# Kernel tuning notes

Hardware: AMD Instinct MI355X
Metric: run time of the kernel (lower is better)

Reference implementation:

```python
import jax, jax.numpy as jnp
import numpy as np

EMB = 1024
N_HEAD = 16
D_K = EMB // N_HEAD


def setup_inputs() -> dict:
    key = jax.random.key(0)
    ks = jax.random.split(key, 11)
    B, S = 4, 2048
    scale = 1.0 / np.sqrt(EMB)
    inp = {
        "q": jax.random.normal(ks[0], (B, S, EMB), jnp.float32),
        "k": jax.random.normal(ks[1], (B, S, EMB), jnp.float32),
        "v": jax.random.normal(ks[2], (B, S, EMB), jnp.float32),
        "Wq": jax.random.normal(ks[3], (EMB, EMB), jnp.float32) * scale,
        "bq": jnp.zeros((EMB,), jnp.float32),
        "Wk": jax.random.normal(ks[4], (EMB, EMB), jnp.float32) * scale,
        "bk": jnp.zeros((EMB,), jnp.float32),
        "Wv": jax.random.normal(ks[5], (EMB, EMB), jnp.float32) * scale,
        "bv": jnp.zeros((EMB,), jnp.float32),
        "Wo": jax.random.normal(ks[6], (EMB, EMB), jnp.float32) * scale,
        "bo": jnp.zeros((EMB,), jnp.float32),
    }
    return inp


def reference(q, k, v, Wq, bq, Wk, bk, Wv, bv, Wo, bo):
    B, S, _ = q.shape
    # project and split heads: [B, H, S, d_k]
    def split(x, W, b):
        y = x @ W.T + b
        return y.reshape(B, -1, N_HEAD, D_K).transpose(0, 2, 1, 3)

    qh = split(q, Wq, bq)
    kh = split(k, Wk, bk)
    vh = split(v, Wv, bv)
    scores = jnp.einsum("bhqd,bhkd->bhqk", qh, kh) / jnp.sqrt(
        jnp.asarray(D_K, qh.dtype))
    attn = jax.nn.softmax(scores, axis=-1)
    out = jnp.einsum("bhqk,bhkd->bhqd", attn, vh)
    out = out.transpose(0, 2, 1, 3).reshape(B, -1, EMB)
    return out @ Wo.T + bo
```

## Files before the change

### kernel.cpp

```cpp
#include <hip/hip_runtime.h>
#include <hip/hip_bf16.h>

#define S_LEN 2048
#define EMB_D 1024
#define NH 16
#define DK 64
#define BATCH 4

typedef __attribute__((ext_vector_type(8))) short short8;
typedef __attribute__((ext_vector_type(4))) float f32x4;
typedef __attribute__((ext_vector_type(8))) unsigned short ushort8;
typedef __attribute__((ext_vector_type(4))) unsigned short ushort4v;
typedef __attribute__((ext_vector_type(4))) unsigned int uint4v;
typedef __attribute__((ext_vector_type(2))) unsigned int uint2v;

__device__ inline unsigned short f2bf(float x) {
    unsigned u = __builtin_bit_cast(unsigned, x);
    u = (u + 0x7fffu + ((u >> 16) & 1u)) >> 16;
    return (unsigned short)u;
}

__device__ inline unsigned cvtpk(float lo, float hi) {
    unsigned r;
    asm("v_cvt_pk_bf16_f32 %0, %1, %2" : "=v"(r) : "v"(lo), "v"(hi));
    return r;
}

typedef const __attribute__((address_space(1))) unsigned int* gas_p;
typedef __attribute__((address_space(3))) unsigned int* las_p;
__device__ inline void gload16(const void* g, void* l) {
    __builtin_amdgcn_global_load_lds((gas_p)g, (las_p)l, 16, 0, 0);
}

struct CvtArgs {
    const float* src[7];
    unsigned short* dst[7];
    int starts[8];
    int ntens;
};

__global__ __launch_bounds__(256) void cvt_all(CvtArgs a) {
    int b = blockIdx.x;
    int t = 0;
#pragma unroll
    for (int i = 1; i < 7; ++i)
        if (i < a.ntens && b >= a.starts[i]) t = i;
    int rel = b - a.starts[t];
    size_t i = (size_t)rel * 2048 + (size_t)threadIdx.x * 8;
    float4 x = *(const float4*)&a.src[t][i];
    float4 y = *(const float4*)&a.src[t][i + 4];
    uint4v w;
    w.x = cvtpk(x.x, x.y); w.y = cvtpk(x.z, x.w);
    w.z = cvtpk(y.x, y.y); w.w = cvtpk(y.z, y.w);
    *(uint4v*)&a.dst[t][i] = w;
}

__global__ __launch_bounds__(256, 4) void gemm_qkv(
    const unsigned short* __restrict__ Aq, const unsigned short* __restrict__ Ak,
    const unsigned short* __restrict__ Av, const unsigned short* __restrict__ Wcat,
    const float* __restrict__ bq, const float* __restrict__ bk, const float* __restrict__ bv,
    unsigned short* __restrict__ Qh, unsigned short* __restrict__ Kh,
    unsigned short* __restrict__ Vt, float qscale)
{
    const int K = EMB_D;
    __shared__ unsigned short As[128][64];
    __shared__ unsigned short Bs[128][64];

    const int tid = threadIdx.x;
    const int lane = tid & 63;
    const int wid = tid >> 6;
    const int wr = wid >> 1, wc = wid & 1;
    const int l15 = lane & 15, l4 = lane >> 4;
    const int lx7 = l15 & 7;

    const int bid = blockIdx.x;
    const int xcd = bid & 7, j = bid >> 3;
    const int tau = j >> 6, jj = j & 63;
    const int bnl = jj & 7;
    const int bm = xcd * 8 + (jj >> 3);

    const unsigned short* Ab = tau == 0 ? Aq : (tau == 1 ? Ak : Av);
    const unsigned short* Bw = Wcat + (size_t)tau * (size_t)EMB_D * EMB_D;
    const float* bias = tau == 0 ? bq : (tau == 1 ? bk : bv);
    const float osc = tau == 0 ? qscale : 1.0f;

    const int srow = lane >> 3;
    const int sgl = lane & 7;

    f32x4 acc[4][4];
#pragma unroll
    for (int m = 0; m < 4; ++m)
#pragma unroll
        for (int n = 0; n < 4; ++n) {
            f32x4 z = {0.f, 0.f, 0.f, 0.f};
            acc[m][n] = z;
        }

    for (int kt = 0; kt < K / 64; ++kt) {
#pragma unroll
        for (int q2 = 0; q2 < 4; ++q2) {
            int r = wid * 32 + q2 * 8 + srow;
            gload16(&Ab[(size_t)(bm * 128 + r) * K + kt * 64 + (sgl ^ srow) * 8],
                    &As[wid * 32 + q2 * 8][0]);
        }
#pragma unroll
        for (int q2 = 0; q2 < 4; ++q2) {
            int r = wid * 32 + q2 * 8 + srow;
            gload16(&Bw[(size_t)(bnl * 128 + r) * K + kt * 64 + (sgl ^ srow) * 8],
                    &Bs[wid * 32 + q2 * 8][0]);
        }
        __syncthreads();
#pragma unroll
        for (int h = 0; h < 2; ++h) {
            short8 af[4], bf[4];
#pragma unroll
            for (int m = 0; m < 4; ++m)
                af[m] = *(const short8*)&As[wr * 64 + m * 16 + l15][((h * 4 + l4) ^ lx7) * 8];
#pragma unroll
            for (int n = 0; n < 4; ++n)
                bf[n] = *(const short8*)&Bs[wc * 64 + n * 16 + l15][((h * 4 + l4) ^ lx7) * 8];
#pragma unroll
            for (int m = 0; m < 4; ++m)
#pragma unroll
                for (int n = 0; n < 4; ++n)
                    acc[m][n] = __builtin_amdgcn_mfma_f32_16x16x32_bf16(af[m], bf[n], acc[m][n], 0, 0, 0);
        }
        __syncthreads();
    }

#pragma unroll
    for (int m = 0; m < 4; ++m) {
#pragma unroll
        for (int n = 0; n < 4; ++n) {
            int gm0 = bm * 128 + wr * 64 + m * 16 + l4 * 4;
            int gn = bnl * 128 + wc * 64 + n * 16 + l15;
            if (tau == 2) {
                int b = gm0 >> 11, s0 = gm0 & 2047;
                int h = gn >> 6, d = gn & 63;
                ushort4v w;
#pragma unroll
                for (int r = 0; r < 4; ++r)
                    w[r] = f2bf(acc[m][n][r] + bias[gn]);
                *(ushort4v*)&Vt[((size_t)(b * NH + h) * DK + d) * S_LEN + s0] = w;
            } else {
                unsigned short* Out = tau == 0 ? Qh : Kh;
#pragma unroll
                for (int r = 0; r < 4; ++r) {
                    int gm = gm0 + r;
                    float val = (acc[m][n][r] + bias[gn]) * osc;
                    int b = gm >> 11, s = gm & 2047;
                    int h = gn >> 6, d = gn & 63;
                    Out[((size_t)(b * NH + h) * S_LEN + s) * DK + d] = f2bf(val);
                }
            }
        }
    }
}

__global__ __launch_bounds__(256, 4) void gemm_o(
    const unsigned short* __restrict__ Ain, const unsigned short* __restrict__ Bw,
    const float* __restrict__ bias, float* __restrict__ Cout)
{
    const int K = EMB_D;
    __shared__ unsigned short As[128][64];
    __shared__ unsigned short Bs[128][64];

    const int tid = threadIdx.x;
    const int lane = tid & 63;
    const int wid = tid >> 6;
    const int wr = wid >> 1, wc = wid & 1;
    const int l15 = lane & 15, l4 = lane >> 4;
    const int lx7 = l15 & 7;

    const int bid = blockIdx.x;
    const int bm = (bid & 7) * 8 + (bid >> 6);
    const int bn = (bid >> 3) & 7;

    const int srow = lane >> 3;
    const int sgl = lane & 7;

    f32x4 acc[4][4];
#pragma unroll
    for (int m = 0; m < 4; ++m)
#pragma unroll
        for (int n = 0; n < 4; ++n) {
            f32x4 z = {0.f, 0.f, 0.f, 0.f};
            acc[m][n] = z;
        }

    for (int kt = 0; kt < K / 64; ++kt) {
#pragma unroll
        for (int q2 = 0; q2 < 4; ++q2) {
            int r = wid * 32 + q2 * 8 + srow;
            gload16(&Ain[(size_t)(bm * 128 + r) * K + kt * 64 + (sgl ^ srow) * 8],
                    &As[wid * 32 + q2 * 8][0]);
        }
#pragma unroll
        for (int q2 = 0; q2 < 4; ++q2) {
            int r = wid * 32 + q2 * 8 + srow;
            gload16(&Bw[(size_t)(bn * 128 + r) * K + kt * 64 + (sgl ^ srow) * 8],
                    &Bs[wid * 32 + q2 * 8][0]);
        }
        __syncthreads();
#pragma unroll
        for (int h = 0; h < 2; ++h) {
            short8 af[4], bf[4];
#pragma unroll
            for (int m = 0; m < 4; ++m)
                af[m] = *(const short8*)&As[wr * 64 + m * 16 + l15][((h * 4 + l4) ^ lx7) * 8];
#pragma unroll
            for (int n = 0; n < 4; ++n)
                bf[n] = *(const short8*)&Bs[wc * 64 + n * 16 + l15][((h * 4 + l4) ^ lx7) * 8];
#pragma unroll
            for (int m = 0; m < 4; ++m)
#pragma unroll
                for (int n = 0; n < 4; ++n)
                    acc[m][n] = __builtin_amdgcn_mfma_f32_16x16x32_bf16(af[m], bf[n], acc[m][n], 0, 0, 0);
        }
        __syncthreads();
    }

#pragma unroll
    for (int m = 0; m < 4; ++m) {
#pragma unroll
        for (int n = 0; n < 4; ++n) {
            int gm0 = bm * 128 + wr * 64 + m * 16 + l4 * 4;
            int gn = bn * 128 + wc * 64 + n * 16 + l15;
#pragma unroll
            for (int r = 0; r < 4; ++r)
                Cout[(size_t)(gm0 + r) * EMB_D + gn] = acc[m][n][r] + bias[gn];
        }
    }
}

template<int A_MODE, int OUT_MODE>
__global__ __launch_bounds__(256) void gemm_bt(
    const void* __restrict__ Aptr, const unsigned short* __restrict__ Bw,
    const float* __restrict__ bias, void* __restrict__ Cout, float oscale)
{
    const int K = EMB_D;
    __shared__ unsigned short As[2][128][64];
    __shared__ unsigned short Bs[2][128][64];

    const int tid = threadIdx.x;
    const int lane = tid & 63;
    const int wid = tid >> 6;
    const int wr = wid >> 1, wc = wid & 1;
    const int l15 = lane & 15, l4 = lane >> 4;
    const int lx7 = l15 & 7;

    const int bid = blockIdx.x;
    const int bm = (bid & 7) * 8 + (bid >> 6);
    const int bn = (bid >> 3) & 7;

    const int srow = lane >> 3;
    const int sgl = lane & 7;

    const float* Af = (const float*)Aptr;
    const unsigned short* Ab = (const unsigned short*)Aptr;

    f32x4 acc[4][4];
#pragma unroll
    for (int m = 0; m < 4; ++m)
#pragma unroll
        for (int n = 0; n < 4; ++n) {
            f32x4 z = {0.f, 0.f, 0.f, 0.f};
            acc[m][n] = z;
        }

    float4 areg[8];

    auto stageB = [&](int c, int kt) {
#pragma unroll
        for (int q2 = 0; q2 < 4; ++q2) {
            int r = wid * 32 + q2 * 8 + srow;
            gload16(&Bw[(size_t)(bn * 128 + r) * K + kt * 64 + (sgl ^ srow) * 8],
                    &Bs[c][wid * 32 + q2 * 8][0]);
        }
    };
    auto stageA1 = [&](int c, int kt) {
#pragma unroll
        for (int q2 = 0; q2 < 4; ++q2) {
            int r = wid * 32 + q2 * 8 + srow;
            gload16(&Ab[(size_t)(bm * 128 + r) * K + kt * 64 + (sgl ^ srow) * 8],
                    &As[c][wid * 32 + q2 * 8][0]);
        }
    };
    auto loadA0 = [&](int kt) {
#pragma unroll
        for (int j = 0; j < 8; ++j) {
            int f = tid + j * 256;
            int r = f >> 4, c4 = f & 15;
            areg[j] = *(const float4*)&Af[(size_t)(bm * 128 + r) * K + kt * 64 + c4 * 4];
        }
    };
    auto writeA0 = [&](int c) {
#pragma unroll
        for (int j = 0; j < 8; ++j) {
            int f = tid + j * 256;
            int r = f >> 4, c4 = f & 15;
            uint2v w;
            w.x = cvtpk(areg[j].x, areg[j].y);
            w.y = cvtpk(areg[j].z, areg[j].w);
            int col = (((c4 >> 1) ^ (r & 7)) << 3) + ((c4 & 1) << 2);
            *(uint2v*)&As[c][r][col] = w;
        }
    };

    if (A_MODE == 0) loadA0(0); else stageA1(0, 0);
    stageB(0, 0);
    if (A_MODE == 0) {
        asm volatile("s_waitcnt vmcnt(0)" ::: "memory");
        writeA0(0);
    }
    __syncthreads();

    for (int kt = 0; kt < K / 64; ++kt) {
        const int c = kt & 1;
        const bool pf = (kt + 1 < K / 64);
        if (pf) {
            if (A_MODE == 0) loadA0(kt + 1); else stageA1(c ^ 1, kt + 1);
            stageB(c ^ 1, kt + 1);
        }
#pragma unroll
        for (int h = 0; h < 2; ++h) {
            short8 af[4], bf[4];
#pragma unroll
            for (int m = 0; m < 4; ++m)
                af[m] = *(const short8*)&As[c][wr * 64 + m * 16 + l15][((h * 4 + l4) ^ lx7) * 8];
#pragma unroll
            for (int n = 0; n < 4; ++n)
                bf[n] = *(const short8*)&Bs[c][wc * 64 + n * 16 + l15][((h * 4 + l4) ^ lx7) * 8];
#pragma unroll
            for (int m = 0; m < 4; ++m)
#pragma unroll
                for (int n = 0; n < 4; ++n)
                    acc[m][n] = __builtin_amdgcn_mfma_f32_16x16x32_bf16(af[m], bf[n], acc[m][n], 0, 0, 0);
        }
        if (pf && A_MODE == 0) {
            asm volatile("s_waitcnt vmcnt(0)" ::: "memory");
            writeA0(c ^ 1);
        }
        __syncthreads();
    }

#pragma unroll
    for (int m = 0; m < 4; ++m) {
#pragma unroll
        for (int n = 0; n < 4; ++n) {
            int gm0 = bm * 128 + wr * 64 + m * 16 + l4 * 4;
            int gn = bn * 128 + wc * 64 + n * 16 + l15;
            if (OUT_MODE == 2) {
                int b = gm0 >> 11, s0 = gm0 & 2047;
                int h = gn >> 6, d = gn & 63;
                ushort4v w;
#pragma unroll
                for (int r = 0; r < 4; ++r)
                    w[r] = f2bf((acc[m][n][r] + bias[gn]) * oscale);
                *(ushort4v*)&((unsigned short*)Cout)[((size_t)(b * NH + h) * DK + d) * S_LEN + s0] = w;
            } else {
#pragma unroll
                for (int r = 0; r < 4; ++r) {
                    int gm = gm0 + r;
                    float val = (acc[m][n][r] + bias[gn]) * oscale;
                    if (OUT_MODE == 1) {
                        int b = gm >> 11, s = gm & 2047;
                        int h = gn >> 6, d = gn & 63;
                        ((unsigned short*)Cout)[((size_t)(b * NH + h) * S_LEN + s) * DK + d] = f2bf(val);
                    } else {
                        ((float*)Cout)[(size_t)gm * EMB_D + gn] = val;
                    }
                }
            }
        }
    }
}

__global__ __launch_bounds__(256, 4) void attn_fwd(
    const unsigned short* __restrict__ Qh, const unsigned short* __restrict__ Kh,
    const unsigned short* __restrict__ Vt, unsigned short* __restrict__ Aout)
{
    __shared__ unsigned short Ks[2][64][64];
    __shared__ unsigned short Vts[2][64][64];

    const int tid = threadIdx.x;
    const int lane = tid & 63;
    const int wid = tid >> 6;
    const int l15 = lane & 15, l4 = lane >> 4;
    const int lx7 = l15 & 7;

    const int bid = blockIdx.x;
    const int swz = (bid & 7) * 128 + (bid >> 3);
    const int bh = swz >> 4, qt = swz & 15;

    const unsigned short* Qb = Qh + (size_t)bh * S_LEN * DK;
    const unsigned short* Kb = Kh + (size_t)bh * S_LEN * DK;
    const unsigned short* Vtb = Vt + (size_t)bh * DK * S_LEN;

    const int srow = lane >> 3;
    const int sgl = lane & 7;

    auto stage = [&](int c, int kt) {
#pragma unroll
        for (int q2 = 0; q2 < 2; ++q2) {
            int q = wid * 2 + q2;
            int rho = q * 8 + srow;
            int kappa = ((rho >> 5) & 1) * 32 + ((rho >> 3) & 1) * 16 +
                        ((rho >> 2) & 1) * 8 + ((rho >> 4) & 1) * 4 + (rho & 3);
            gload16(&Kb[(size_t)(kt * 64 + kappa) * DK + (sgl ^ srow) * 8],
                    &Ks[c][q * 8][0]);
            gload16(&Vtb[(size_t)rho * S_LEN + kt * 64 + (sgl ^ srow) * 8],
                    &Vts[c][q * 8][0]);
        }
    };

    short8 qf[2][2];
#pragma unroll
    for (int m = 0; m < 2; ++m) {
        int qrow = qt * 128 + wid * 32 + m * 16 + l15;
#pragma unroll
        for (int h = 0; h < 2; ++h)
            qf[m][h] = *(const short8*)&Qb[(size_t)qrow * DK + h * 32 + l4 * 8];
    }

    f32x4 ot[2][5];
#pragma unroll
    for (int m = 0; m < 2; ++m)
#pragma unroll
        for (int n = 0; n < 5; ++n) {
            f32x4 z = {0.f, 0.f, 0.f, 0.f};
            ot[m][n] = z;
        }

    short8 ones;
#pragma unroll
    for (int e = 0; e < 8; ++e) ones[e] = (short)0x3F80;

    const f32x4 fz = {0.f, 0.f, 0.f, 0.f};

    stage(0, 0);
    __syncthreads();

    for (int kt = 0; kt < S_LEN / 64; ++kt) {
        const int c = kt & 1;
        if (kt + 1 < S_LEN / 64) stage(c ^ 1, kt + 1);

        f32x4 st[2][4];
        __builtin_amdgcn_s_setprio(1);
#pragma unroll
        for (int kb = 0; kb < 4; ++kb) {
            short8 kf0 = *(const short8*)&Ks[c][kb * 16 + l15][((0 + l4) ^ lx7) * 8];
#pragma unroll
            for (int m = 0; m < 2; ++m)
                st[m][kb] = __builtin_amdgcn_mfma_f32_16x16x32_bf16(kf0, qf[m][0], fz, 0, 0, 0);
            short8 kf1 = *(const short8*)&Ks[c][kb * 16 + l15][((4 + l4) ^ lx7) * 8];
#pragma unroll
            for (int m = 0; m < 2; ++m)
                st[m][kb] = __builtin_amdgcn_mfma_f32_16x16x32_bf16(kf1, qf[m][1], st[m][kb], 0, 0, 0);
        }
        __builtin_amdgcn_s_setprio(0);

        short8 pa[2][2];
#pragma unroll
        for (int m = 0; m < 2; ++m) {
#pragma unroll
            for (int kb = 0; kb < 4; ++kb)
#pragma unroll
                for (int r = 0; r < 4; ++r)
                    st[m][kb][r] = __builtin_amdgcn_exp2f(st[m][kb][r]);
#pragma unroll
            for (int h = 0; h < 2; ++h) {
                uint4v w;
                w.x = cvtpk(st[m][2 * h][0], st[m][2 * h][1]);
                w.y = cvtpk(st[m][2 * h][2], st[m][2 * h][3]);
                w.z = cvtpk(st[m][2 * h + 1][0], st[m][2 * h + 1][1]);
                w.w = cvtpk(st[m][2 * h + 1][2], st[m][2 * h + 1][3]);
                pa[m][h] = __builtin_bit_cast(short8, w);
            }
        }

        __builtin_amdgcn_s_setprio(1);
#pragma unroll
        for (int n = 0; n < 4; ++n)
#pragma unroll
            for (int h = 0; h < 2; ++h) {
                short8 vb = *(const short8*)&Vts[c][n * 16 + l15][((h * 4 + l4) ^ lx7) * 8];
#pragma unroll
                for (int m = 0; m < 2; ++m)
                    ot[m][n] = __builtin_amdgcn_mfma_f32_16x16x32_bf16(pa[m][h], vb, ot[m][n], 0, 0, 0);
            }
#pragma unroll
        for (int h = 0; h < 2; ++h)
#pragma unroll
            for (int m = 0; m < 2; ++m)
                ot[m][4] = __builtin_amdgcn_mfma_f32_16x16x32_bf16(pa[m][h], ones, ot[m][4], 0, 0, 0);
        __builtin_amdgcn_s_setprio(0);
        __syncthreads();
    }

    const int b = bh >> 4, hh = bh & 15;
#pragma unroll
    for (int m = 0; m < 2; ++m) {
#pragma unroll
        for (int r = 0; r < 4; ++r) {
            float inv = 1.0f / ot[m][4][r];
            int s = qt * 128 + wid * 32 + m * 16 + l4 * 4 + r;
#pragma unroll
            for (int n = 0; n < 4; ++n) {
                int d = n * 16 + l15;
                Aout[((size_t)(b * S_LEN + s)) * EMB_D + hh * DK + d] = f2bf(ot[m][n][r] * inv);
            }
        }
    }
}

extern "C" void kernel_launch(void* const* d_in, const int* in_sizes, int n_in,
                              void* d_out, int out_size, void* d_ws, size_t ws_size,
                              hipStream_t stream) {
    const float* q  = (const float*)d_in[0];
    const float* k  = (const float*)d_in[1];
    const float* v  = (const float*)d_in[2];
    const float* Wq = (const float*)d_in[3];
    const float* bq = (const float*)d_in[4];
    const float* Wk = (const float*)d_in[5];
    const float* bk = (const float*)d_in[6];
    const float* Wv = (const float*)d_in[7];
    const float* bv = (const float*)d_in[8];
    const float* Wo = (const float*)d_in[9];
    const float* bo = (const float*)d_in[10];

    const size_t seg = (size_t)BATCH * NH * S_LEN * DK;
    const size_t wseg = (size_t)EMB_D * EMB_D;
    unsigned short* Qh = (unsigned short*)d_ws;
    unsigned short* Kh = Qh + seg;
    unsigned short* Vh = Kh + seg;
    unsigned short* Ao = Vh + seg;
    unsigned short* Wqb = Ao + seg;
    unsigned short* Wkb = Wqb + wseg;
    unsigned short* Wvb = Wkb + wseg;
    unsigned short* Wob = Wvb + wseg;
    unsigned short* qb = Wob + wseg;
    unsigned short* kb2 = qb + seg;
    unsigned short* vb2 = kb2 + seg;

    const size_t full_elems = seg * 7 + wseg * 4;
    const bool full = ws_size >= full_elems * 2;

    const float qscale = 0.18033688011112042f;

    const int WBLK = (int)(wseg / 2048);
    const int SBLK = (int)(seg / 2048);

    CvtArgs ca;
    ca.src[0] = Wq;  ca.dst[0] = Wqb;
    ca.src[1] = Wk;  ca.dst[1] = Wkb;
    ca.src[2] = Wv;  ca.dst[2] = Wvb;
    ca.src[3] = Wo;  ca.dst[3] = Wob;
    ca.starts[0] = 0;
    ca.starts[1] = WBLK;
    ca.starts[2] = WBLK * 2;
    ca.starts[3] = WBLK * 3;
    int nb = WBLK * 4;
    if (full) {
        ca.src[4] = q; ca.dst[4] = qb;
        ca.src[5] = k; ca.dst[5] = kb2;
        ca.src[6] = v; ca.dst[6] = vb2;
        ca.starts[4] = nb;
        ca.starts[5] = nb + SBLK;
        ca.starts[6] = nb + SBLK * 2;
        ca.ntens = 7;
        nb += SBLK * 3;
    } else {
        ca.src[4] = ca.src[5] = ca.src[6] = Wq;
        ca.dst[4] = ca.dst[5] = ca.dst[6] = Wqb;
        ca.starts[4] = ca.starts[5] = ca.starts[6] = nb;
        ca.ntens = 4;
    }
    ca.starts[7] = nb;
    cvt_all<<<nb, 256, 0, stream>>>(ca);

    if (full) {
        gemm_qkv<<<1536, 256, 0, stream>>>(qb, kb2, vb2, Wqb, bq, bk, bv,
                                           Qh, Kh, Vh, qscale);
    } else {
        gemm_bt<0, 1><<<512, 256, 0, stream>>>((const void*)q, Wqb, bq, (void*)Qh, qscale);
        gemm_bt<0, 1><<<512, 256, 0, stream>>>((const void*)k, Wkb, bk, (void*)Kh, 1.0f);
        gemm_bt<0, 2><<<512, 256, 0, stream>>>((const void*)v, Wvb, bv, (void*)Vh, 1.0f);
    }

    attn_fwd<<<1024, 256, 0, stream>>>(Qh, Kh, Vh, Ao);

    gemm_o<<<512, 256, 0, stream>>>(Ao, Wob, bo, (float*)d_out);
}
```

Measured before the change: 178.2 us.

## Fuse fp32-to-bf16 activation conversion into QKV projection GEMM loads

The QKV GEMM now reads the fp32 q/k/v activations directly, converts them to bf16 in registers, and writes them into the swizzled LDS tile. The separate conversion pass and its bf16 staging buffers for the activations go away, which removes a full write and re-read of those tensors. In exchange the GEMM's A-tile loads double in bytes, go through registers instead of direct-to-LDS loads, and wait on all outstanding loads before the LDS store, which may reduce overlap. It also lowers the workspace needed for the fused path.

```diff
diff --git a/kernel.cpp b/kernel.cpp
--- a/kernel.cpp
+++ b/kernel.cpp
@@ -56,8 +56,8 @@
 }
 
 __global__ __launch_bounds__(256, 4) void gemm_qkv(
-    const unsigned short* __restrict__ Aq, const unsigned short* __restrict__ Ak,
-    const unsigned short* __restrict__ Av, const unsigned short* __restrict__ Wcat,
+    const float* __restrict__ Aq, const float* __restrict__ Ak,
+    const float* __restrict__ Av, const unsigned short* __restrict__ Wcat,
     const float* __restrict__ bq, const float* __restrict__ bk, const float* __restrict__ bv,
     unsigned short* __restrict__ Qh, unsigned short* __restrict__ Kh,
     unsigned short* __restrict__ Vt, float qscale)
@@ -79,7 +79,7 @@
     const int bnl = jj & 7;
     const int bm = xcd * 8 + (jj >> 3);
 
-    const unsigned short* Ab = tau == 0 ? Aq : (tau == 1 ? Ak : Av);
+    const float* Af = tau == 0 ? Aq : (tau == 1 ? Ak : Av);
     const unsigned short* Bw = Wcat + (size_t)tau * (size_t)EMB_D * EMB_D;
     const float* bias = tau == 0 ? bq : (tau == 1 ? bk : bv);
     const float osc = tau == 0 ? qscale : 1.0f;
@@ -97,17 +97,29 @@
         }
 
     for (int kt = 0; kt < K / 64; ++kt) {
-#pragma unroll
-        for (int q2 = 0; q2 < 4; ++q2) {
-            int r = wid * 32 + q2 * 8 + srow;
-            gload16(&Ab[(size_t)(bm * 128 + r) * K + kt * 64 + (sgl ^ srow) * 8],
-                    &As[wid * 32 + q2 * 8][0]);
+        float4 areg[8];
+#pragma unroll
+        for (int jj2 = 0; jj2 < 8; ++jj2) {
+            int f = tid + jj2 * 256;
+            int r = f >> 4, c4 = f & 15;
+            areg[jj2] = *(const float4*)&Af[(size_t)(bm * 128 + r) * K + kt * 64 + c4 * 4];
         }
 #pragma unroll
         for (int q2 = 0; q2 < 4; ++q2) {
             int r = wid * 32 + q2 * 8 + srow;
             gload16(&Bw[(size_t)(bnl * 128 + r) * K + kt * 64 + (sgl ^ srow) * 8],
                     &Bs[wid * 32 + q2 * 8][0]);
+        }
+        asm volatile("s_waitcnt vmcnt(0)" ::: "memory");
+#pragma unroll
+        for (int jj2 = 0; jj2 < 8; ++jj2) {
+            int f = tid + jj2 * 256;
+            int r = f >> 4, c4 = f & 15;
+            uint2v w;
+            w.x = cvtpk(areg[jj2].x, areg[jj2].y);
+            w.y = cvtpk(areg[jj2].z, areg[jj2].w);
+            int col = (((c4 >> 1) ^ (r & 7)) << 3) + ((c4 & 1) << 2);
+            *(uint2v*)&As[r][col] = w;
         }
         __syncthreads();
 #pragma unroll
@@ -539,17 +551,13 @@
     unsigned short* Wkb = Wqb + wseg;
     unsigned short* Wvb = Wkb + wseg;
     unsigned short* Wob = Wvb + wseg;
-    unsigned short* qb = Wob + wseg;
-    unsigned short* kb2 = qb + seg;
-    unsigned short* vb2 = kb2 + seg;
-
-    const size_t full_elems = seg * 7 + wseg * 4;
-    const bool full = ws_size >= full_elems * 2;
+
+    const size_t need_elems = seg * 4 + wseg * 4;
+    const bool full = ws_size >= need_elems * 2;
 
     const float qscale = 0.18033688011112042f;
 
     const int WBLK = (int)(wseg / 2048);
-    const int SBLK = (int)(seg / 2048);
 
     CvtArgs ca;
     ca.src[0] = Wq;  ca.dst[0] = Wqb;
@@ -561,26 +569,15 @@
     ca.starts[2] = WBLK * 2;
     ca.starts[3] = WBLK * 3;
     int nb = WBLK * 4;
-    if (full) {
-        ca.src[4] = q; ca.dst[4] = qb;
-        ca.src[5] = k; ca.dst[5] = kb2;
-        ca.src[6] = v; ca.dst[6] = vb2;
-        ca.starts[4] = nb;
-        ca.starts[5] = nb + SBLK;
-        ca.starts[6] = nb + SBLK * 2;
-        ca.ntens = 7;
-        nb += SBLK * 3;
-    } else {
-        ca.src[4] = ca.src[5] = ca.src[6] = Wq;
-        ca.dst[4] = ca.dst[5] = ca.dst[6] = Wqb;
-        ca.starts[4] = ca.starts[5] = ca.starts[6] = nb;
-        ca.ntens = 4;
-    }
+    ca.src[4] = ca.src[5] = ca.src[6] = Wq;
+    ca.dst[4] = ca.dst[5] = ca.dst[6] = Wqb;
+    ca.starts[4] = ca.starts[5] = ca.starts[6] = nb;
+    ca.ntens = 4;
     ca.starts[7] = nb;
     cvt_all<<<nb, 256, 0, stream>>>(ca);
 
     if (full) {
-        gemm_qkv<<<1536, 256, 0, stream>>>(qb, kb2, vb2, Wqb, bq, bk, bv,
+        gemm_qkv<<<1536, 256, 0, stream>>>(q, k, v, Wqb, bq, bk, bv,
                                            Qh, Kh, Vh, qscale);
     } else {
         gemm_bt<0, 1><<<512, 256, 0, stream>>>((const void*)q, Wqb, bq, (void*)Qh, qscale);
```

Result: slower. 214.9 us (+20.6%).

## Rewrite fused QKV GEMM as 256x256 tile, 8-wave, double-buffered ping-pong pipeline

Applied to the files above, without the earlier changes.

Replaces the 128x128 single-buffered QKV projection GEMM with a 256x256-tile kernel using 512 threads (8 waves), double-buffered LDS, and phased loads interleaved with MFMA blocks under explicit barriers and s_setprio. Global-to-LDS loads for the next k-tiles are issued between MFMA quarters, aiming to hide memory latency and raise per-block data reuse. The grid shrinks from 1536 to 384 blocks, and LDS use grows to 128KB per block, so fewer blocks fit per CU. Occupancy and tail-wave balance across CUs may suffer.

```diff
diff --git a/kernel.cpp b/kernel.cpp
--- a/kernel.cpp
+++ b/kernel.cpp
@@ -55,7 +55,36 @@
     *(uint4v*)&a.dst[t][i] = w;
 }
 
-__global__ __launch_bounds__(256, 4) void gemm_qkv(
+
+#define LDSA8(c, mq)                                                               \
+    _Pragma("unroll") for (int mf = 0; mf < 4; ++mf)                               \
+    _Pragma("unroll") for (int kk = 0; kk < 2; ++kk)                               \
+        af[mf][kk] = *(const short8*)&As[c][wr * 128 + (mq) * 64 + mf * 16 + l15]  \
+                                         [((kk * 4 + l4) ^ lx7) * 8];
+
+#define LDSB8(c, nh)                                                               \
+    _Pragma("unroll") for (int nf = 0; nf < 2; ++nf)                               \
+    _Pragma("unroll") for (int kk = 0; kk < 2; ++kk)                               \
+        bf[(nh) * 2 + nf][kk] = *(const short8*)&Bs[c][wc * 64 + ((nh) * 2 + nf) * 16 + l15] \
+                                                     [((kk * 4 + l4) ^ lx7) * 8];
+
+#define MMA_Q(mq, nh)                                                              \
+    __builtin_amdgcn_s_setprio(1);                                                 \
+    _Pragma("unroll") for (int mf = 0; mf < 4; ++mf)                               \
+    _Pragma("unroll") for (int nf = 0; nf < 2; ++nf)                               \
+    _Pragma("unroll") for (int kk = 0; kk < 2; ++kk)                               \
+        acc[(mq) * 4 + mf][(nh) * 2 + nf] = __builtin_amdgcn_mfma_f32_16x16x32_bf16( \
+            af[mf][kk], bf[(nh) * 2 + nf][kk], acc[(mq) * 4 + mf][(nh) * 2 + nf], 0, 0, 0); \
+    __builtin_amdgcn_s_setprio(0);
+
+#define PH_OPEN                                                                    \
+    __builtin_amdgcn_s_barrier();                                                  \
+    asm volatile("s_waitcnt lgkmcnt(0)" ::: "memory");                             \
+    __builtin_amdgcn_sched_barrier(0);
+
+#define PH_CLOSE __builtin_amdgcn_s_barrier();
+
+__global__ __launch_bounds__(512, 2) void gemm_qkv8(
     const unsigned short* __restrict__ Aq, const unsigned short* __restrict__ Ak,
     const unsigned short* __restrict__ Av, const unsigned short* __restrict__ Wcat,
     const float* __restrict__ bq, const float* __restrict__ bk, const float* __restrict__ bv,
@@ -63,21 +92,22 @@
     unsigned short* __restrict__ Vt, float qscale)
 {
     const int K = EMB_D;
-    __shared__ unsigned short As[128][64];
-    __shared__ unsigned short Bs[128][64];
+    __shared__ unsigned short As[2][256][64];
+    __shared__ unsigned short Bs[2][256][64];
 
     const int tid = threadIdx.x;
     const int lane = tid & 63;
     const int wid = tid >> 6;
-    const int wr = wid >> 1, wc = wid & 1;
+    const int wr = wid >> 2;
+    const int wc = wid & 3;
     const int l15 = lane & 15, l4 = lane >> 4;
     const int lx7 = l15 & 7;
 
     const int bid = blockIdx.x;
     const int xcd = bid & 7, j = bid >> 3;
-    const int tau = j >> 6, jj = j & 63;
-    const int bnl = jj & 7;
-    const int bm = xcd * 8 + (jj >> 3);
+    const int tau = j >> 4, jj = j & 15;
+    const int bnl = jj & 3;
+    const int bm = xcd * 4 + (jj >> 2);
 
     const unsigned short* Ab = tau == 0 ? Aq : (tau == 1 ? Ak : Av);
     const unsigned short* Bw = Wcat + (size_t)tau * (size_t)EMB_D * EMB_D;
@@ -87,53 +117,78 @@
     const int srow = lane >> 3;
     const int sgl = lane & 7;
 
-    f32x4 acc[4][4];
-#pragma unroll
-    for (int m = 0; m < 4; ++m)
+    auto stA = [&](int c, int h, int kt) {
+#pragma unroll
+        for (int q2 = 0; q2 < 2; ++q2) {
+            int rb = h * 128 + wid * 16 + q2 * 8;
+            gload16(&Ab[(size_t)(bm * 256 + rb + srow) * K + kt * 64 + (sgl ^ srow) * 8],
+                    &As[c][rb][0]);
+        }
+    };
+    auto stB = [&](int c, int h, int kt) {
+#pragma unroll
+        for (int q2 = 0; q2 < 2; ++q2) {
+            int rb = h * 128 + wid * 16 + q2 * 8;
+            gload16(&Bw[(size_t)(bnl * 256 + rb + srow) * K + kt * 64 + (sgl ^ srow) * 8],
+                    &Bs[c][rb][0]);
+        }
+    };
+
+    f32x4 acc[8][4];
+#pragma unroll
+    for (int m = 0; m < 8; ++m)
 #pragma unroll
         for (int n = 0; n < 4; ++n) {
             f32x4 z = {0.f, 0.f, 0.f, 0.f};
             acc[m][n] = z;
         }
-
-    for (int kt = 0; kt < K / 64; ++kt) {
-#pragma unroll
-        for (int q2 = 0; q2 < 4; ++q2) {
-            int r = wid * 32 + q2 * 8 + srow;
-            gload16(&Ab[(size_t)(bm * 128 + r) * K + kt * 64 + (sgl ^ srow) * 8],
-                    &As[wid * 32 + q2 * 8][0]);
-        }
-#pragma unroll
-        for (int q2 = 0; q2 < 4; ++q2) {
-            int r = wid * 32 + q2 * 8 + srow;
-            gload16(&Bw[(size_t)(bnl * 128 + r) * K + kt * 64 + (sgl ^ srow) * 8],
-                    &Bs[wid * 32 + q2 * 8][0]);
-        }
-        __syncthreads();
-#pragma unroll
-        for (int h = 0; h < 2; ++h) {
-            short8 af[4], bf[4];
-#pragma unroll
-            for (int m = 0; m < 4; ++m)
-                af[m] = *(const short8*)&As[wr * 64 + m * 16 + l15][((h * 4 + l4) ^ lx7) * 8];
-#pragma unroll
-            for (int n = 0; n < 4; ++n)
-                bf[n] = *(const short8*)&Bs[wc * 64 + n * 16 + l15][((h * 4 + l4) ^ lx7) * 8];
-#pragma unroll
-            for (int m = 0; m < 4; ++m)
-#pragma unroll
-                for (int n = 0; n < 4; ++n)
-                    acc[m][n] = __builtin_amdgcn_mfma_f32_16x16x32_bf16(af[m], bf[n], acc[m][n], 0, 0, 0);
-        }
-        __syncthreads();
-    }
-
-#pragma unroll
-    for (int m = 0; m < 4; ++m) {
+    short8 af[4][2];
+    short8 bf[4][2];
+
+    stA(0, 0, 0); stA(0, 1, 0); stB(0, 0, 0); stB(0, 1, 0);
+    stB(1, 0, 1); stB(1, 1, 1);
+    asm volatile("s_waitcnt vmcnt(4)" ::: "memory");
+    __builtin_amdgcn_s_barrier();
+
+    for (int i = 0; i < 8; ++i) {
+        const int t1 = 2 * i + 1, t2 = 2 * i + 2, t3 = 2 * i + 3;
+        const bool pf = (i < 7);
+        LDSA8(0, 0); LDSB8(0, 0);
+        stA(1, 0, t1);
+        PH_OPEN; MMA_Q(0, 0); PH_CLOSE;
+        LDSB8(0, 1);
+        stA(1, 1, t1);
+        PH_OPEN; MMA_Q(0, 1); PH_CLOSE;
+        LDSA8(0, 1);
+        if (pf) stB(0, 0, t2);
+        PH_OPEN; MMA_Q(1, 0); PH_CLOSE;
+        if (pf) stB(0, 1, t2);
+        PH_OPEN; MMA_Q(1, 1);
+        if (pf) { asm volatile("s_waitcnt vmcnt(4)" ::: "memory"); }
+        else    { asm volatile("s_waitcnt vmcnt(0)" ::: "memory"); }
+        PH_CLOSE;
+        LDSA8(1, 0); LDSB8(1, 0);
+        if (pf) stA(0, 0, t2);
+        PH_OPEN; MMA_Q(0, 0); PH_CLOSE;
+        LDSB8(1, 1);
+        if (pf) stA(0, 1, t2);
+        PH_OPEN; MMA_Q(0, 1); PH_CLOSE;
+        LDSA8(1, 1);
+        if (pf) stB(1, 0, t3);
+        PH_OPEN; MMA_Q(1, 0); PH_CLOSE;
+        if (pf) stB(1, 1, t3);
+        PH_OPEN; MMA_Q(1, 1);
+        if (pf) { asm volatile("s_waitcnt vmcnt(4)" ::: "memory"); }
+        else    { asm volatile("s_waitcnt vmcnt(0)" ::: "memory"); }
+        PH_CLOSE;
+    }
+
+#pragma unroll
+    for (int m = 0; m < 8; ++m) {
 #pragma unroll
         for (int n = 0; n < 4; ++n) {
-            int gm0 = bm * 128 + wr * 64 + m * 16 + l4 * 4;
-            int gn = bnl * 128 + wc * 64 + n * 16 + l15;
+            int gm0 = bm * 256 + wr * 128 + m * 16 + l4 * 4;
+            int gn = bnl * 256 + wc * 64 + n * 16 + l15;
             if (tau == 2) {
                 int b = gm0 >> 11, s0 = gm0 & 2047;
                 int h = gn >> 6, d = gn & 63;
@@ -288,20 +343,20 @@
     };
     auto loadA0 = [&](int kt) {
 #pragma unroll
-        for (int j = 0; j < 8; ++j) {
-            int f = tid + j * 256;
+        for (int j2 = 0; j2 < 8; ++j2) {
+            int f = tid + j2 * 256;
             int r = f >> 4, c4 = f & 15;
-            areg[j] = *(const float4*)&Af[(size_t)(bm * 128 + r) * K + kt * 64 + c4 * 4];
+            areg[j2] = *(const float4*)&Af[(size_t)(bm * 128 + r) * K + kt * 64 + c4 * 4];
         }
     };
     auto writeA0 = [&](int c) {
 #pragma unroll
-        for (int j = 0; j < 8; ++j) {
-            int f = tid + j * 256;
+        for (int j2 = 0; j2 < 8; ++j2) {
+            int f = tid + j2 * 256;
             int r = f >> 4, c4 = f & 15;
             uint2v w;
-            w.x = cvtpk(areg[j].x, areg[j].y);
-            w.y = cvtpk(areg[j].z, areg[j].w);
+            w.x = cvtpk(areg[j2].x, areg[j2].y);
+            w.y = cvtpk(areg[j2].z, areg[j2].w);
             int col = (((c4 >> 1) ^ (r & 7)) << 3) + ((c4 & 1) << 2);
             *(uint2v*)&As[c][r][col] = w;
         }
@@ -580,7 +635,7 @@
     cvt_all<<<nb, 256, 0, stream>>>(ca);
 
     if (full) {
-        gemm_qkv<<<1536, 256, 0, stream>>>(qb, kb2, vb2, Wqb, bq, bk, bv,
+        gemm_qkv8<<<384, 512, 0, stream>>>(qb, kb2, vb2, Wqb, bq, bk, bv,
                                            Qh, Kh, Vh, qscale);
     } else {
         gemm_bt<0, 1><<<512, 256, 0, stream>>>((const void*)q, Wqb, bq, (void*)Qh, qscale);
```

After: 199.6 us. 12.1% more time.
